# Optimization experiments

Hardware: AMD Instinct MI355X
Metric: run time of the kernel (lower is better)

The kernel has to match this reference:

```python
import jax, jax.numpy as jnp
import numpy as np

N = 50000      # nodes
E = 800000     # edges (before self loops)
H = 2          # attention heads
CH = 64        # per-head hidden channels
IN = 128       # input features
OUT = 64       # output channels
EPS = 1e-5     # batchnorm eps
SLOPE = 0.2    # LeakyReLU negative slope


def _gat_conv(x, src, dst, W, a_src, a_dst, b, concat):
    # x: [N, Fin]; W: [Fin, H*C]; a_src/a_dst: [H, C]
    n = x.shape[0]
    h = (x @ W).reshape(n, H, -1)                       # [N, H, C]
    al_s = (h * a_src).sum(-1)                          # [N, H]
    al_d = (h * a_dst).sum(-1)                          # [N, H]
    e = al_s[src] + al_d[dst]                           # [E, H]
    e = jnp.where(e > 0, e, SLOPE * e)                  # LeakyReLU
    # softmax over edges grouped by destination node
    m = jax.ops.segment_max(e, dst, num_segments=n)
    ex = jnp.exp(e - m[dst])
    den = jax.ops.segment_sum(ex, dst, num_segments=n)
    alpha = ex / (den[dst] + 1e-16)                     # [E, H]
    out = jax.ops.segment_sum(h[src] * alpha[:, :, None], dst, num_segments=n)
    out = out.reshape(n, -1) if concat else out.mean(axis=1)
    return out + b


def _batchnorm(x, g, be):
    mu = x.mean(axis=0)
    var = x.var(axis=0)  # biased, as torch BN uses in training
    return (x - mu) * jax.lax.rsqrt(var + EPS) * g + be


def setup_inputs() -> dict:
    key = jax.random.key(0)
    ks = jax.random.split(key, 18)
    s = 0.1
    inp = {
        "x": jax.random.normal(ks[0], (N, IN), jnp.float32),
        "edge_index": jax.random.randint(ks[1], (2, E), 0, N, jnp.int64),
        # layer 0: IN -> H*CH (concat)
        "W0": jax.random.normal(ks[2], (IN, H * CH), jnp.float32) * s,
        "a_src0": jax.random.normal(ks[3], (H, CH), jnp.float32) * s,
        "a_dst0": jax.random.normal(ks[4], (H, CH), jnp.float32) * s,
        "b0": jnp.zeros((H * CH,), jnp.float32),
        "g0": jnp.ones((H * CH,), jnp.float32),
        "be0": jnp.zeros((H * CH,), jnp.float32),
        # layer 1: H*CH -> H*CH (concat)
        "W1": jax.random.normal(ks[5], (H * CH, H * CH), jnp.float32) * s,
        "a_src1": jax.random.normal(ks[6], (H, CH), jnp.float32) * s,
        "a_dst1": jax.random.normal(ks[7], (H, CH), jnp.float32) * s,
        "b1": jnp.zeros((H * CH,), jnp.float32),
        "g1": jnp.ones((H * CH,), jnp.float32),
        "be1": jnp.zeros((H * CH,), jnp.float32),
        # layer 2: H*CH -> OUT, concat=False (mean over heads)
        "W2": jax.random.normal(ks[8], (H * CH, H * OUT), jnp.float32) * s,
        "a_src2": jax.random.normal(ks[9], (H, OUT), jnp.float32) * s,
        "a_dst2": jax.random.normal(ks[10], (H, OUT), jnp.float32) * s,
        "b2": jnp.zeros((OUT,), jnp.float32),
    }
    return inp


def reference(x, edge_index, W0, a_src0, a_dst0, b0, g0, be0,
              W1, a_src1, a_dst1, b1, g1, be1,
              W2, a_src2, a_dst2, b2):
    # add self loops (PyG GATConv default)
    loop = jnp.arange(N, dtype=edge_index.dtype)
    src = jnp.concatenate([edge_index[0], loop])
    dst = jnp.concatenate([edge_index[1], loop])

    h = _gat_conv(x, src, dst, W0, a_src0, a_dst0, b0, concat=True)
    h = jax.nn.relu(_batchnorm(h, g0, be0))
    # dropout: eval mode (identity)
    h = _gat_conv(h, src, dst, W1, a_src1, a_dst1, b1, concat=True)
    h = jax.nn.relu(_batchnorm(h, g1, be1))
    out = _gat_conv(h, src, dst, W2, a_src2, a_dst2, b2, concat=False)
    return out
```

## Files before the change

### kernel.cpp

```cpp
#include <hip/hip_runtime.h>


#define N_NODES 50000
#define N_EDGES 800000
#define ET (N_EDGES + N_NODES)
#define FDIM 128
#define SLOPE 0.2f
#define BN_EPS 1e-5f
#define SCAN_NB 196
#define HIST_NB 3321
#define RPK_NB 216
#define LOG2E 1.44269504088896340736f
#define WSTRIDE 18432

typedef __attribute__((ext_vector_type(8))) short bf16x8;
typedef __attribute__((ext_vector_type(4))) float f32x4;
typedef __attribute__((ext_vector_type(8))) unsigned short u16x8;

__device__ __forceinline__ unsigned short f2bf(float f) {
  unsigned u = __float_as_uint(f);
  u = u + 0x7fffu + ((u >> 16) & 1u);
  return (unsigned short)(u >> 16);
}
__device__ __forceinline__ unsigned packbf(float lo, float hi) {
  return ((unsigned)f2bf(hi) << 16) | (unsigned)f2bf(lo);
}
__device__ __forceinline__ float bflo(unsigned p) { return __uint_as_float(p << 16); }
__device__ __forceinline__ float bfhi(unsigned p) { return __uint_as_float(p & 0xffff0000u); }

__global__ __launch_bounds__(256) void build_pre(const int* __restrict__ dst,
                                                 int* __restrict__ counts,
                                                 int* __restrict__ rank,
                                                 const float* __restrict__ W0,
                                                 const float* __restrict__ W1,
                                                 const float* __restrict__ W2,
                                                 const float* __restrict__ as0,
                                                 const float* __restrict__ as1,
                                                 const float* __restrict__ as2,
                                                 const float* __restrict__ ad0,
                                                 const float* __restrict__ ad1,
                                                 const float* __restrict__ ad2,
                                                 unsigned short* __restrict__ Wr) {
  int bid = blockIdx.x;
  if (bid < HIST_NB) {
    int i = bid * 256 + threadIdx.x;
    if (i >= ET) return;
    int d = (i < N_EDGES) ? dst[i] : i - N_EDGES;
    rank[i] = atomicAdd(&counts[d], 1);
    return;
  }
  int i = (bid - HIST_NB) * 256 + threadIdx.x;
  if (i >= 3 * WSTRIDE) return;
  int L = i / WSTRIDE, rem = i % WSTRIDE;
  int t  = rem >> 11;
  int ks = (rem >> 9) & 3;
  int ln = (rem >> 3) & 63;
  int j  = rem & 7;
  int k  = ks * 32 + (ln >> 4) * 8 + j;
  const float* W = (L == 0) ? W0 : ((L == 1) ? W1 : W2);
  float val;
  if (t < 8) {
    int col = t * 16 + (ln & 15);
    val = W[k * 128 + col];
  } else {
    int cl = ln & 15;
    if (cl < 4) {
      int head = cl & 1;
      const float* a = (cl < 2) ? ((L == 0) ? as0 : (L == 1) ? as1 : as2)
                                : ((L == 0) ? ad0 : (L == 1) ? ad1 : ad2);
      float s = 0.f;
      const float* wrow = W + k * 128 + head * 64;
      const float* ah = a + head * 64;
#pragma unroll 8
      for (int c = 0; c < 64; ++c) s = fmaf(wrow[c], ah[c], s);
      val = s * LOG2E;
    } else {
      val = 0.f;
    }
  }
  Wr[i] = f2bf(val);
}


__global__ __launch_bounds__(256) void scan_blk(const int* __restrict__ counts,
                                                int* __restrict__ rowptr,
                                                int* __restrict__ partials) {
  int i = blockIdx.x * 256 + threadIdx.x;
  int lane = threadIdx.x & 63, wv = threadIdx.x >> 6;
  int c = (i < N_NODES) ? counts[i] : 0;
  int v = c;
#pragma unroll
  for (int off = 1; off < 64; off <<= 1) {
    int u = __shfl_up(v, off);
    if (lane >= off) v += u;
  }
  __shared__ int wsum[4];
  if (lane == 63) wsum[wv] = v;
  __syncthreads();
  int add = 0;
  for (int w = 0; w < wv; ++w) add += wsum[w];
  if (i < N_NODES) rowptr[i] = v - c + add;
  if (threadIdx.x == 255) partials[blockIdx.x] = add + v;
}

__global__ __launch_bounds__(256) void scan_fin(int* __restrict__ rowptr,
                                                const int* __restrict__ partials) {
  __shared__ int sh[256];
  int t = threadIdx.x;
  sh[t] = (t < (int)blockIdx.x && t < SCAN_NB) ? partials[t] : 0;
  __syncthreads();
#pragma unroll
  for (int off = 128; off > 0; off >>= 1) {
    if (t < off) sh[t] += sh[t + off];
    __syncthreads();
  }
  int base = sh[0];
  int i = blockIdx.x * 256 + t;
  if (i < N_NODES) rowptr[i] += base;
  if (i == 0) rowptr[N_NODES] = ET;
}

__global__ __launch_bounds__(256) void scatter_pos(const int* __restrict__ src,
                                                   const int* __restrict__ dst,
                                                   const int* __restrict__ rowptr,
                                                   const int* __restrict__ rank,
                                                   int* __restrict__ csr_src) {
  int i = blockIdx.x * 256 + threadIdx.x;
  if (i >= ET) return;
  int d, s;
  if (i < N_EDGES) { d = dst[i]; s = src[i]; } else { d = s = i - N_EDGES; }
  csr_src[rowptr[d] + rank[i]] = s;
}

__global__ __launch_bounds__(128) void bn_fin(float* __restrict__ part,
                                              const float* __restrict__ g,
                                              const float* __restrict__ be,
                                              float* __restrict__ lsbuf) {
  int t = threadIdx.x;
  float s = 0.f, q = 0.f;
#pragma unroll
  for (int k = 0; k < 32; ++k) {
    s += part[k * 256 + t];
    q += part[k * 256 + 128 + t];
    part[k * 256 + t] = 0.f;
    part[k * 256 + 128 + t] = 0.f;
  }
  float mu  = s * (1.f / N_NODES);
  float var = q * (1.f / N_NODES) - mu * mu;
  float sc  = rsqrtf(var + BN_EPS) * g[t];
  lsbuf[t]       = sc;
  lsbuf[128 + t] = be[t] - mu * sc;
}

__global__ __launch_bounds__(256) void gemm_mfma(const void* __restrict__ Xin,
                                                 const unsigned short* __restrict__ WrL,
                                                 const float* __restrict__ lsbuf,
                                                 unsigned short* __restrict__ Hbf,
                                                 float* __restrict__ als,
                                                 float* __restrict__ ald,
                                                 int inBF) {
  __shared__ unsigned short lds[4][16][128];
  __shared__ float ls_scale[128], ls_shift[128];
  int lane = threadIdx.x & 63;
  int wv   = threadIdx.x >> 6;

  if (inBF) {
    int t = threadIdx.x;
    if (t < 128) {
      ls_scale[t] = lsbuf[t];
      ls_shift[t] = lsbuf[128 + t];
    }
    __syncthreads();
  }

  int row0 = blockIdx.x * 64 + wv * 16;
  int gidx = lane & 15;
  int quad = lane >> 4;
  int rA   = row0 + gidx;
  int rAc  = rA < N_NODES ? rA : N_NODES - 1;
  int koff = quad * 8;

  f32x4 acc[9] = {};
#pragma unroll
  for (int ks = 0; ks < 4; ++ks) {
    int cb = ks * 32 + koff;
    float xv[8];
    if (inBF) {
      const uint4* xr = (const uint4*)((const unsigned*)Xin + (size_t)rAc * 64 + (cb >> 1));
      uint4 xa = *xr;
      xv[0] = bflo(xa.x); xv[1] = bfhi(xa.x);
      xv[2] = bflo(xa.y); xv[3] = bfhi(xa.y);
      xv[4] = bflo(xa.z); xv[5] = bfhi(xa.z);
      xv[6] = bflo(xa.w); xv[7] = bfhi(xa.w);
    } else {
      const float4* xr = (const float4*)((const float*)Xin + (size_t)rAc * FDIM + cb);
      float4 xa = xr[0], xb = xr[1];
      xv[0] = xa.x; xv[1] = xa.y; xv[2] = xa.z; xv[3] = xa.w;
      xv[4] = xb.x; xv[5] = xb.y; xv[6] = xb.z; xv[7] = xb.w;
    }
    bf16x8 afrag;
    if (inBF) {
#pragma unroll
      for (int j = 0; j < 8; ++j) {
        int c = cb + j;
        float v = fmaf(xv[j], ls_scale[c], ls_shift[c]);
        v = v > 0.f ? v : 0.f;
        afrag[j] = (short)f2bf(v);
      }
    } else {
#pragma unroll
      for (int j = 0; j < 8; ++j) afrag[j] = (short)f2bf(xv[j]);
    }
#pragma unroll
    for (int t = 0; t < 9; ++t) {
      bf16x8 bfrag = *(const bf16x8*)(WrL + ((size_t)((t * 4 + ks) * 64 + lane)) * 8);
      acc[t] = __builtin_amdgcn_mfma_f32_16x16x32_bf16(afrag, bfrag, acc[t], 0, 0, 0);
    }
  }

  if (gidx < 4) {
    float* dp = (gidx < 2) ? als : ald;
    int hd = gidx & 1;
#pragma unroll
    for (int r = 0; r < 4; ++r) {
      int row = row0 + quad * 4 + r;
      if (row < N_NODES) dp[row * 2 + hd] = acc[8][r];
    }
  }

#pragma unroll
  for (int t = 0; t < 8; ++t)
#pragma unroll
    for (int r = 0; r < 4; ++r)
      lds[wv][quad * 4 + r][t * 16 + gidx] = f2bf(acc[t][r]);
  __syncthreads();
#pragma unroll
  for (int it = 0; it < 4; ++it) {
    int rloc = it * 4 + quad;
    int row = row0 + rloc;
    if (row < N_NODES)
      *(u16x8*)(Hbf + (size_t)row * FDIM + gidx * 8) = *(u16x8*)&lds[wv][rloc][gidx * 8];
  }
}

__global__ __launch_bounds__(256) void fused_agg(const int* __restrict__ rowptr,
                                                 const int* __restrict__ csr_src,
                                                 const unsigned* __restrict__ H2,
                                                 const float* __restrict__ als,
                                                 const float* __restrict__ ald,
                                                 unsigned* __restrict__ Abf,
                                                 float* __restrict__ out,
                                                 const float* __restrict__ b2,
                                                 float* __restrict__ part,
                                                 int mode) {
  int lane = threadIdx.x & 63;
  int sl   = lane & 31;
  int half = lane >> 5;
  int head = sl >> 4;
  int gw = (blockIdx.x * 256 + threadIdx.x) >> 6;
  int n = gw * 2 + half;

  int beg = rowptr[n];
  int end = rowptr[n + 1];
  int deg = end - beg;
  int degm1 = deg - 1;
  float advh = ald[(size_t)n * 2 + head];

  int dm = max(deg, __shfl_xor(deg, 32));
  dm = __builtin_amdgcn_readfirstlane(dm);
  int nb = (dm + 7) >> 3;

  float av[8]; uint2 ha[8]; int saB[8];
#pragma unroll
  for (int i = 0; i < 8; ++i) {
    int t = i < degm1 ? i : degm1;
    int s = csr_src[beg + t];
    av[i] = als[(size_t)s * 2 + head];
    ha[i] = *(const uint2*)(H2 + (size_t)s * 64 + 2 * sl);
  }
#pragma unroll
  for (int i = 0; i < 8; ++i) {
    int t = 8 + i; t = t < degm1 ? t : degm1;
    saB[i] = csr_src[beg + t];
  }

  float l = 0.f, o0 = 0.f, o1 = 0.f, o2 = 0.f, o3 = 0.f;
  int rem = deg;

#define STEP(i) { \
    float v_ = av[i] + advh; \
    v_ = fmaxf(v_, SLOPE * v_); \
    v_ = (i < rem) ? v_ : -1000.f; \
    float e_ = exp2f(v_); \
    l += e_; \
    o0 = fmaf(e_, bflo(ha[i].x), o0); \
    o1 = fmaf(e_, bfhi(ha[i].x), o1); \
    o2 = fmaf(e_, bflo(ha[i].y), o2); \
    o3 = fmaf(e_, bfhi(ha[i].y), o3); }

  for (int b = 0; b + 1 < nb; ++b) {
    float an[8]; uint2 hn[8];
#pragma unroll
    for (int i = 0; i < 8; ++i) {
      an[i] = als[(size_t)saB[i] * 2 + head];
      hn[i] = *(const uint2*)(H2 + (size_t)saB[i] * 64 + 2 * sl);
    }
    int nxt = (b + 2) * 8;
#pragma unroll
    for (int i = 0; i < 8; ++i) {
      int t = nxt + i; t = t < degm1 ? t : degm1;
      saB[i] = csr_src[beg + t];
    }
    STEP(0); STEP(1); STEP(2); STEP(3); STEP(4); STEP(5); STEP(6); STEP(7);
    rem -= 8;
#pragma unroll
    for (int i = 0; i < 8; ++i) { av[i] = an[i]; ha[i] = hn[i]; }
  }
  STEP(0); STEP(1); STEP(2); STEP(3); STEP(4); STEP(5); STEP(6); STEP(7);
#undef STEP

  float inv = 1.f / (l + 1e-16f);
  o0 *= inv; o1 *= inv; o2 *= inv; o3 *= inv;

  if (mode == 0) {
    uint2 pk = { packbf(o0, o1), packbf(o2, o3) };
    *(uint2*)(Abf + (size_t)n * 64 + 2 * sl) = pk;
    __shared__ float sh[4][2][32][4];
    int wv = threadIdx.x >> 6;
    float4 quad = { o0, o1, o2, o3 };
    *(float4*)&sh[wv][half][sl][0] = quad;
    __syncthreads();
    if (threadIdx.x < 128) {
      int c = threadIdx.x;
      int q = c >> 2, r = c & 3;
      float a = 0.f, asq = 0.f;
#pragma unroll
      for (int w = 0; w < 4; ++w)
#pragma unroll
        for (int hh = 0; hh < 2; ++hh) {
          float v = sh[w][hh][q][r];
          a += v; asq += v * v;
        }
      float* slot = part + (blockIdx.x & 31) * 256;
      atomicAdd(&slot[c], a);
      atomicAdd(&slot[128 + c], asq);
    }
  } else {
    float p0 = __shfl_xor(o0, 16);
    float p1 = __shfl_xor(o1, 16);
    float p2 = __shfl_xor(o2, 16);
    float p3 = __shfl_xor(o3, 16);
    if (head == 0) {
      int c = sl * 4;
      float4 bv = *(const float4*)(b2 + c);
      float4 ov = { 0.5f * (o0 + p0) + bv.x, 0.5f * (o1 + p1) + bv.y,
                    0.5f * (o2 + p2) + bv.z, 0.5f * (o3 + p3) + bv.w };
      *(float4*)(out + (size_t)n * 64 + c) = ov;
    }
  }
}

extern "C" void kernel_launch(void* const* d_in, const int* in_sizes, int n_in,
                              void* d_out, int out_size, void* d_ws, size_t ws_size,
                              hipStream_t stream) {
  const float* x  = (const float*)d_in[0];
  const int*   ei = (const int*)d_in[1];
  const int* src = ei;
  const int* dst = ei + N_EDGES;

  const float* W[3]    = {(const float*)d_in[2],  (const float*)d_in[8],  (const float*)d_in[14]};
  const float* asrc[3] = {(const float*)d_in[3],  (const float*)d_in[9],  (const float*)d_in[15]};
  const float* adst[3] = {(const float*)d_in[4],  (const float*)d_in[10], (const float*)d_in[16]};
  const float* g[2]    = {(const float*)d_in[6],  (const float*)d_in[12]};
  const float* be[2]   = {(const float*)d_in[7],  (const float*)d_in[13]};
  const float* b2      = (const float*)d_in[17];

  int*   counts   = (int*)d_ws;
  float* part     = (float*)(counts + 50048);
  int*   rowptr   = (int*)(part + 8192);
  int*   partials = rowptr + 50048;
  int*   rank     = partials + 256;
  int*   csr_src  = rank + 850048;
  float* lsbuf    = (float*)(csr_src + 850048);
  float* als      = lsbuf + 256;
  float* ald      = als + 100096;
  unsigned short* Wr  = (unsigned short*)(ald + 100096);
  unsigned short* Hbf = Wr + 3 * WSTRIDE + 128;
  unsigned* Abf   = (unsigned*)(Hbf + (size_t)N_NODES * FDIM);

  hipMemsetAsync(counts, 0, (50048 + 8192) * sizeof(int), stream);
  build_pre<<<HIST_NB + RPK_NB, 256, 0, stream>>>(
      dst, counts, rank, W[0], W[1], W[2],
      asrc[0], asrc[1], asrc[2], adst[0], adst[1], adst[2], Wr);
  scan_blk<<<SCAN_NB, 256, 0, stream>>>(counts, rowptr, partials);
  scan_fin<<<SCAN_NB, 256, 0, stream>>>(rowptr, partials);
  scatter_pos<<<(ET + 255) / 256, 256, 0, stream>>>(src, dst, rowptr, rank, csr_src);

  const int gemm_grid = (N_NODES + 63) / 64;
  const int agg_grid  = N_NODES / 8;

  for (int L = 0; L < 3; ++L) {
    const void* fin = (L == 0) ? (const void*)x : (const void*)Abf;
    int inBF = (L > 0);
    gemm_mfma<<<gemm_grid, 256, 0, stream>>>(fin, Wr + (size_t)L * WSTRIDE, lsbuf,
                                             Hbf, als, ald, inBF);
    fused_agg<<<agg_grid, 256, 0, stream>>>(rowptr, csr_src, (const unsigned*)Hbf,
                                            als, ald, Abf, (float*)d_out, b2, part,
                                            (L == 2) ? 2 : 0);
    if (L < 2)
      bn_fin<<<1, 128, 0, stream>>>(part, g[L], be[L], lsbuf);
  }
}
```

Baseline: 330.1 us.

## Split each node's edge list across two wavefronts and merge partial sums in LDS

The aggregation kernel now assigns two wavefronts per node pair, each processing half of the incoming edges, and combines the partial softmax numerators and denominators through shared memory before normalising. The grid is doubled to match. This shortens the serial dependent-gather chain per wave and raises the number of waves available to hide memory latency. In exchange it adds an extra LDS round trip and block barrier, and half the waves sit idle during the epilogue. The unnormalised exp2 without a max-subtraction is carried over unchanged.

```diff
diff --git a/kernel.cpp b/kernel.cpp
--- a/kernel.cpp
+++ b/kernel.cpp
@@ -257,35 +257,40 @@
   int sl   = lane & 31;
   int half = lane >> 5;
   int head = sl >> 4;
-  int gw = (blockIdx.x * 256 + threadIdx.x) >> 6;
-  int n = gw * 2 + half;
+  int wv   = threadIdx.x >> 6;
+  int hseg = wv & 1;
+  int pair = (blockIdx.x << 1) | (wv >> 1);
+  int n = pair * 2 + half;
 
   int beg = rowptr[n];
   int end = rowptr[n + 1];
   int deg = end - beg;
-  int degm1 = deg - 1;
+  int hd  = (deg + 1) >> 1;
+  int lbeg = beg + hseg * hd;
+  int len  = hseg ? (deg - hd) : hd;
+  int last = end - 1;
   float advh = ald[(size_t)n * 2 + head];
 
-  int dm = max(deg, __shfl_xor(deg, 32));
-  dm = __builtin_amdgcn_readfirstlane(dm);
-  int nb = (dm + 7) >> 3;
+  int lm = max(len, __shfl_xor(len, 32));
+  lm = __builtin_amdgcn_readfirstlane(lm);
+  int nb = (lm + 7) >> 3;
 
   float av[8]; uint2 ha[8]; int saB[8];
 #pragma unroll
   for (int i = 0; i < 8; ++i) {
-    int t = i < degm1 ? i : degm1;
-    int s = csr_src[beg + t];
+    int idx = lbeg + i; idx = idx > last ? last : idx;
+    int s = csr_src[idx];
     av[i] = als[(size_t)s * 2 + head];
     ha[i] = *(const uint2*)(H2 + (size_t)s * 64 + 2 * sl);
   }
 #pragma unroll
   for (int i = 0; i < 8; ++i) {
-    int t = 8 + i; t = t < degm1 ? t : degm1;
-    saB[i] = csr_src[beg + t];
+    int idx = lbeg + 8 + i; idx = idx > last ? last : idx;
+    saB[i] = csr_src[idx];
   }
 
   float l = 0.f, o0 = 0.f, o1 = 0.f, o2 = 0.f, o3 = 0.f;
-  int rem = deg;
+  int rem = len;
 
 #define STEP(i) { \
     float v_ = av[i] + advh; \
@@ -305,11 +310,11 @@
       an[i] = als[(size_t)saB[i] * 2 + head];
       hn[i] = *(const uint2*)(H2 + (size_t)saB[i] * 64 + 2 * sl);
     }
-    int nxt = (b + 2) * 8;
+    int nxt = lbeg + (b + 2) * 8;
 #pragma unroll
     for (int i = 0; i < 8; ++i) {
-      int t = nxt + i; t = t < degm1 ? t : degm1;
-      saB[i] = csr_src[beg + t];
+      int idx = nxt + i; idx = idx > last ? last : idx;
+      saB[i] = csr_src[idx];
     }
     STEP(0); STEP(1); STEP(2); STEP(3); STEP(4); STEP(5); STEP(6); STEP(7);
     rem -= 8;
@@ -319,43 +324,55 @@
   STEP(0); STEP(1); STEP(2); STEP(3); STEP(4); STEP(5); STEP(6); STEP(7);
 #undef STEP
 
-  float inv = 1.f / (l + 1e-16f);
-  o0 *= inv; o1 *= inv; o2 *= inv; o3 *= inv;
+  __shared__ float sho[4][2][32][4];
+  __shared__ float shl[4][2][32];
+  float4 pq = { o0, o1, o2, o3 };
+  *(float4*)&sho[wv][half][sl][0] = pq;
+  shl[wv][half][sl] = l;
+  __syncthreads();
+
+  if (hseg == 0) {
+    float4 po = *(const float4*)&sho[wv ^ 1][half][sl][0];
+    float pl = shl[wv ^ 1][half][sl];
+    float L = l + pl;
+    float inv = 1.f / (L + 1e-16f);
+    float f0 = (o0 + po.x) * inv;
+    float f1 = (o1 + po.y) * inv;
+    float f2 = (o2 + po.z) * inv;
+    float f3 = (o3 + po.w) * inv;
+
+    if (mode == 0) {
+      uint2 pk = { packbf(f0, f1), packbf(f2, f3) };
+      *(uint2*)(Abf + (size_t)n * 64 + 2 * sl) = pk;
+      float4 fq = { f0, f1, f2, f3 };
+      *(float4*)&sho[wv][half][sl][0] = fq;
+    } else {
+      float p0 = __shfl_xor(f0, 16);
+      float p1 = __shfl_xor(f1, 16);
+      float p2 = __shfl_xor(f2, 16);
+      float p3 = __shfl_xor(f3, 16);
+      if (head == 0) {
+        int c = sl * 4;
+        float4 bv = *(const float4*)(b2 + c);
+        float4 ov = { 0.5f * (f0 + p0) + bv.x, 0.5f * (f1 + p1) + bv.y,
+                      0.5f * (f2 + p2) + bv.z, 0.5f * (f3 + p3) + bv.w };
+        *(float4*)(out + (size_t)n * 64 + c) = ov;
+      }
+    }
+  }
 
   if (mode == 0) {
-    uint2 pk = { packbf(o0, o1), packbf(o2, o3) };
-    *(uint2*)(Abf + (size_t)n * 64 + 2 * sl) = pk;
-    __shared__ float sh[4][2][32][4];
-    int wv = threadIdx.x >> 6;
-    float4 quad = { o0, o1, o2, o3 };
-    *(float4*)&sh[wv][half][sl][0] = quad;
     __syncthreads();
     if (threadIdx.x < 128) {
       int c = threadIdx.x;
       int q = c >> 2, r = c & 3;
-      float a = 0.f, asq = 0.f;
-#pragma unroll
-      for (int w = 0; w < 4; ++w)
-#pragma unroll
-        for (int hh = 0; hh < 2; ++hh) {
-          float v = sh[w][hh][q][r];
-          a += v; asq += v * v;
-        }
+      float v00 = sho[0][0][q][r], v01 = sho[0][1][q][r];
+      float v20 = sho[2][0][q][r], v21 = sho[2][1][q][r];
+      float a   = v00 + v01 + v20 + v21;
+      float asq = v00 * v00 + v01 * v01 + v20 * v20 + v21 * v21;
       float* slot = part + (blockIdx.x & 31) * 256;
       atomicAdd(&slot[c], a);
       atomicAdd(&slot[128 + c], asq);
-    }
-  } else {
-    float p0 = __shfl_xor(o0, 16);
-    float p1 = __shfl_xor(o1, 16);
-    float p2 = __shfl_xor(o2, 16);
-    float p3 = __shfl_xor(o3, 16);
-    if (head == 0) {
-      int c = sl * 4;
-      float4 bv = *(const float4*)(b2 + c);
-      float4 ov = { 0.5f * (o0 + p0) + bv.x, 0.5f * (o1 + p1) + bv.y,
-                    0.5f * (o2 + p2) + bv.z, 0.5f * (o3 + p3) + bv.w };
-      *(float4*)(out + (size_t)n * 64 + c) = ov;
     }
   }
 }
@@ -397,7 +414,7 @@
   scatter_pos<<<(ET + 255) / 256, 256, 0, stream>>>(src, dst, rowptr, rank, csr_src);
 
   const int gemm_grid = (N_NODES + 63) / 64;
-  const int agg_grid  = N_NODES / 8;
+  const int agg_grid  = N_NODES / 4;
 
   for (int L = 0; L < 3; ++L) {
     const void* fin = (L == 0) ? (const void*)x : (const void*)Abf;
```

Result: slower. 361.1 us (+9.4%).
